# Performance work log

Hardware: AMD Instinct MI355X
Metric: run time of the kernel (lower is better)

Reference implementation:

```python
import jax, jax.numpy as jnp
import numpy as np

NEG_SLOPE = 0.2
EPS = 1e-16


def setup_inputs() -> dict:
    key = jax.random.key(0)
    k = jax.random.split(key, 6)
    N, K, D_IN, D_OUT = 20000, 32, 256, 256
    nodes = jax.random.normal(k[0], (N, D_IN), dtype=jnp.float32)
    neighbors = jax.random.normal(k[1], (N, K, D_IN), dtype=jnp.float32)
    # xavier-uniform-ish scales for faithfulness to init_params
    lim_w = float(np.sqrt(6.0 / (D_IN + D_OUT)))
    W = jax.random.uniform(k[2], (D_OUT, D_IN), minval=-lim_w, maxval=lim_w, dtype=jnp.float32)
    lim_a = float(np.sqrt(6.0 / (1 + D_OUT)))
    a_src = jax.random.uniform(k[3], (D_OUT,), minval=-lim_a, maxval=lim_a, dtype=jnp.float32)
    a_tgt = jax.random.uniform(k[4], (D_OUT,), minval=-lim_a, maxval=lim_a, dtype=jnp.float32)
    bias = jnp.zeros((D_OUT,), dtype=jnp.float32)
    return {"nodes": nodes, "neighbors": neighbors, "W": W, "a_src": a_src, "a_tgt": a_tgt, "bias": bias}


def reference(nodes, neighbors, W, a_src, a_tgt, bias):
    # GAT layer (num_of_heads=1), eval mode (dropout = identity).
    # nodes: [N, D_in], neighbors: [N, K, D_in]
    nodes_proj = nodes @ W.T                              # [N, D_out]
    scores_t = nodes_proj @ a_tgt                         # [N]
    neigh_proj = jnp.einsum('nkf,of->nko', neighbors, W)  # [N, K, D_out]
    scores_s = neigh_proj @ a_src                         # [N, K]
    e = scores_s + scores_t[:, None]                      # per-edge raw score
    e = jnp.where(e >= 0, e, NEG_SLOPE * e)               # leakyReLU(0.2)
    exp_e = jnp.exp(e)                                    # original uses raw exp (no max-subtract)
    attn = exp_e / (jnp.sum(exp_e, axis=1, keepdims=True) + EPS)  # [N, K]
    out = jnp.einsum('nk,nko->no', attn, neigh_proj)      # weighted sum over neighbors
    out = out + bias
    return jax.nn.elu(out)                                # activation = ELU
```

## Files before the change

### kernel.cpp

```cpp
#include <hip/hip_runtime.h>
#include <hip/hip_bf16.h>
#include <math.h>

#define D 256
#define KNB 32
#define NEG_SLOPE 0.2f

#define PART_OFF 53280
#define AGG_OFF  69664

using bfrag = __attribute__((ext_vector_type(8))) short;
using ffrag = __attribute__((ext_vector_type(4))) float;
using f32x4 = __attribute__((ext_vector_type(4))) float;

__device__ __forceinline__ unsigned short f2bf(float x) {
    __hip_bfloat16 h = __float2bfloat16(x);
    return *reinterpret_cast<unsigned short*>(&h);
}

__global__ __launch_bounds__(256) void prep1_kernel(
    const float* __restrict__ W, const float* __restrict__ a_src,
    const float* __restrict__ a_tgt, float* __restrict__ ws)
{
    int t = threadIdx.x;
    int b = blockIdx.x;
    if (b < 64) {
        float4 v = reinterpret_cast<const float4*>(W)[b * 256 + t];
        ushort4 u;
        u.x = f2bf(v.x); u.y = f2bf(v.y); u.z = f2bf(v.z); u.w = f2bf(v.w);
        reinterpret_cast<ushort4*>(ws + 512)[b * 256 + t] = u;
    } else {
        int bb = b - 64;
        float ps = 0.f, pt = 0.f;
        #pragma unroll
        for (int oo = 0; oo < 8; ++oo) {
            int o = bb * 8 + oo;
            float wv = W[o * D + t];
            ps = fmaf(a_src[o], wv, ps);
            pt = fmaf(a_tgt[o], wv, pt);
        }
        ws[PART_OFF + bb * 256 + t]        = ps;
        ws[PART_OFF + 8192 + bb * 256 + t] = pt;
    }
}

__global__ __launch_bounds__(256) void prep2_kernel(float* __restrict__ ws)
{
    int t = threadIdx.x;
    float s = 0.f, g = 0.f;
    #pragma unroll
    for (int j = 0; j < 32; ++j) {
        s += ws[PART_OFF + j * 256 + t];
        g += ws[PART_OFF + 8192 + j * 256 + t];
    }
    ws[t]     = s;
    ws[D + t] = g;
}

__global__ __launch_bounds__(256) void scores_t_kernel(
    const float* __restrict__ nodes, const float* __restrict__ ws,
    float* __restrict__ scores_t, int N)
{
    int wid  = threadIdx.x >> 6;
    int lane = threadIdx.x & 63;
    int n = blockIdx.x * 4 + wid;
    if (n >= N) return;
    f32x4 v = __builtin_nontemporal_load(
        reinterpret_cast<const f32x4*>(nodes + (size_t)n * D) + lane);
    float4 w = reinterpret_cast<const float4*>(ws + D)[lane];
    float s = v.x * w.x + v.y * w.y + v.z * w.z + v.w * w.w;
    #pragma unroll
    for (int off = 1; off < 64; off <<= 1) s += __shfl_xor(s, off);
    if (lane == 0) scores_t[n] = s;
}

__device__ __forceinline__ float xreduce8(const float* p, int lane)
{
    bool b0 = lane & 1, b1 = lane & 2, b2 = lane & 4;
    float s0_0 = (b0 ? p[1] : p[0]) + __shfl_xor(b0 ? p[0] : p[1], 1);
    float s0_1 = (b0 ? p[3] : p[2]) + __shfl_xor(b0 ? p[2] : p[3], 1);
    float s0_2 = (b0 ? p[5] : p[4]) + __shfl_xor(b0 ? p[4] : p[5], 1);
    float s0_3 = (b0 ? p[7] : p[6]) + __shfl_xor(b0 ? p[6] : p[7], 1);
    float s1_0 = (b1 ? s0_1 : s0_0) + __shfl_xor(b1 ? s0_0 : s0_1, 2);
    float s1_1 = (b1 ? s0_3 : s0_2) + __shfl_xor(b1 ? s0_2 : s0_3, 2);
    float s2   = (b2 ? s1_1 : s1_0) + __shfl_xor(b2 ? s1_0 : s1_1, 4);
    s2 += __shfl_xor(s2, 8);
    s2 += __shfl_xor(s2, 16);
    s2 += __shfl_xor(s2, 32);
    return s2;
}

__global__ __launch_bounds__(256) void attn_agg_kernel(
    const float* __restrict__ neighbors, const float* __restrict__ ws,
    const float* __restrict__ scores_t, unsigned short* __restrict__ aggbf, int N)
{
    __shared__ float spA[KNB], spB[KNB];
    __shared__ float wsumA[4], wsumB[4];
    __shared__ __align__(16) float4 part2A[4][64];
    __shared__ __align__(16) float4 part2B[4][64];

    const int t    = threadIdx.x;
    const int lane = t & 63;
    const int w    = t >> 6;
    const int nA   = blockIdx.x * 2;
    const bool hasB = (nA + 1 < N);
    const int nB   = hasB ? nA + 1 : nA;

    const float4 wsv = reinterpret_cast<const float4*>(ws)[lane];
    const float stA = scores_t[nA];
    const float stB = scores_t[nB];

    const f32x4* tA = reinterpret_cast<const f32x4*>(neighbors + (size_t)nA * (KNB * D));
    const f32x4* tB = reinterpret_cast<const f32x4*>(neighbors + (size_t)nB * (KNB * D));

    f32x4 vA[8], vB[8];
    #pragma unroll
    for (int i = 0; i < 8; ++i)
        vA[i] = __builtin_nontemporal_load(tA + (8 * w + i) * 64 + lane);
    #pragma unroll
    for (int i = 0; i < 8; ++i)
        vB[i] = __builtin_nontemporal_load(tB + (8 * w + i) * 64 + lane);

    {
        float p[8];
        #pragma unroll
        for (int i = 0; i < 8; ++i)
            p[i] = fmaf(vA[i].x, wsv.x, fmaf(vA[i].y, wsv.y,
                   fmaf(vA[i].z, wsv.z, vA[i].w * wsv.w)));
        float s2 = xreduce8(p, lane);
        float e = s2 + stA; e = (e >= 0.f) ? e : NEG_SLOPE * e;
        float x = __expf(e);
        float d = x + __shfl_xor(x, 1);
        d += __shfl_xor(d, 2);
        d += __shfl_xor(d, 4);
        if (lane < 8) spA[8 * w + lane] = x;
        if (lane == 0) wsumA[w] = d;
    }
    {
        float p[8];
        #pragma unroll
        for (int i = 0; i < 8; ++i)
            p[i] = fmaf(vB[i].x, wsv.x, fmaf(vB[i].y, wsv.y,
                   fmaf(vB[i].z, wsv.z, vB[i].w * wsv.w)));
        float s2 = xreduce8(p, lane);
        float e = s2 + stB; e = (e >= 0.f) ? e : NEG_SLOPE * e;
        float x = __expf(e);
        float d = x + __shfl_xor(x, 1);
        d += __shfl_xor(d, 2);
        d += __shfl_xor(d, 4);
        if (lane < 8) spB[8 * w + lane] = x;
        if (lane == 0) wsumB[w] = d;
    }
    __syncthreads();

    {
        float xw[8];
        #pragma unroll
        for (int i = 0; i < 8; ++i) xw[i] = spA[8 * w + i];
        float4 acc = make_float4(0.f, 0.f, 0.f, 0.f);
        #pragma unroll
        for (int i = 0; i < 8; ++i) {
            acc.x = fmaf(xw[i], vA[i].x, acc.x);
            acc.y = fmaf(xw[i], vA[i].y, acc.y);
            acc.z = fmaf(xw[i], vA[i].z, acc.z);
            acc.w = fmaf(xw[i], vA[i].w, acc.w);
        }
        part2A[w][lane] = acc;
    }
    {
        float xw[8];
        #pragma unroll
        for (int i = 0; i < 8; ++i) xw[i] = spB[8 * w + i];
        float4 acc = make_float4(0.f, 0.f, 0.f, 0.f);
        #pragma unroll
        for (int i = 0; i < 8; ++i) {
            acc.x = fmaf(xw[i], vB[i].x, acc.x);
            acc.y = fmaf(xw[i], vB[i].y, acc.y);
            acc.z = fmaf(xw[i], vB[i].z, acc.z);
            acc.w = fmaf(xw[i], vB[i].w, acc.w);
        }
        part2B[w][lane] = acc;
    }
    __syncthreads();

    if (w == 0) {
        float4 q0 = part2A[0][lane], q1 = part2A[1][lane];
        float4 q2 = part2A[2][lane], q3 = part2A[3][lane];
        float inv = 1.f / (wsumA[0] + wsumA[1] + wsumA[2] + wsumA[3] + 1e-16f);
        float4 r;
        r.x = (q0.x + q1.x + q2.x + q3.x) * inv;
        r.y = (q0.y + q1.y + q2.y + q3.y) * inv;
        r.z = (q0.z + q1.z + q2.z + q3.z) * inv;
        r.w = (q0.w + q1.w + q2.w + q3.w) * inv;
        ushort4 u;
        u.x = f2bf(r.x); u.y = f2bf(r.y); u.z = f2bf(r.z); u.w = f2bf(r.w);
        reinterpret_cast<ushort4*>(aggbf + (size_t)nA * D)[lane] = u;
    } else if (w == 1 && hasB) {
        float4 q0 = part2B[0][lane], q1 = part2B[1][lane];
        float4 q2 = part2B[2][lane], q3 = part2B[3][lane];
        float inv = 1.f / (wsumB[0] + wsumB[1] + wsumB[2] + wsumB[3] + 1e-16f);
        float4 r;
        r.x = (q0.x + q1.x + q2.x + q3.x) * inv;
        r.y = (q0.y + q1.y + q2.y + q3.y) * inv;
        r.z = (q0.z + q1.z + q2.z + q3.z) * inv;
        r.w = (q0.w + q1.w + q2.w + q3.w) * inv;
        ushort4 u;
        u.x = f2bf(r.x); u.y = f2bf(r.y); u.z = f2bf(r.z); u.w = f2bf(r.w);
        reinterpret_cast<ushort4*>(aggbf + (size_t)nB * D)[lane] = u;
    }
}

__global__ __launch_bounds__(64) void out_gemm_kernel(
    const unsigned short* __restrict__ aggbf,
    const unsigned short* __restrict__ wbf,
    const float* __restrict__ bias, float* __restrict__ out, int N)
{
    int l = threadIdx.x;
    int m0 = blockIdx.x * 16;
    if (m0 >= N) return;
    int lr = l & 15, lk = l >> 4;

    ffrag acc[16];
    #pragma unroll
    for (int nf = 0; nf < 16; ++nf) acc[nf] = ffrag{0.f, 0.f, 0.f, 0.f};

    #pragma unroll
    for (int ks = 0; ks < 8; ++ks) {
        bfrag a = *reinterpret_cast<const bfrag*>(
            aggbf + (size_t)(m0 + lr) * D + ks * 32 + lk * 8);
        #pragma unroll
        for (int nf = 0; nf < 16; ++nf) {
            bfrag b = *reinterpret_cast<const bfrag*>(
                wbf + (size_t)(nf * 16 + lr) * D + ks * 32 + lk * 8);
            acc[nf] = __builtin_amdgcn_mfma_f32_16x16x32_bf16(a, b, acc[nf], 0, 0, 0);
        }
    }

    #pragma unroll
    for (int nf = 0; nf < 16; ++nf) {
        int col = nf * 16 + lr;
        float bv = bias[col];
        #pragma unroll
        for (int r = 0; r < 4; ++r) {
            int m = m0 + lk * 4 + r;
            float x = acc[nf][r] + bv;
            x = (x > 0.f) ? x : expm1f(x);
            out[(size_t)m * D + col] = x;
        }
    }
}

extern "C" void kernel_launch(void* const* d_in, const int* in_sizes, int n_in,
                              void* d_out, int out_size, void* d_ws, size_t ws_size,
                              hipStream_t stream) {
    const float* nodes     = (const float*)d_in[0];
    const float* neighbors = (const float*)d_in[1];
    const float* W         = (const float*)d_in[2];
    const float* a_src     = (const float*)d_in[3];
    const float* a_tgt     = (const float*)d_in[4];
    const float* bias      = (const float*)d_in[5];
    float* out = (float*)d_out;
    float* ws  = (float*)d_ws;

    int N = in_sizes[0] / D;
    unsigned short* wbf   = (unsigned short*)(ws + 512);
    float* scores_t       = ws + 33280;
    unsigned short* aggbf = (unsigned short*)(ws + AGG_OFF);

    hipLaunchKernelGGL(prep1_kernel, dim3(96), dim3(256), 0, stream,
                       W, a_src, a_tgt, ws);
    hipLaunchKernelGGL(prep2_kernel, dim3(1), dim3(256), 0, stream, ws);
    hipLaunchKernelGGL(scores_t_kernel, dim3((N + 3) / 4), dim3(256), 0, stream,
                       nodes, ws, scores_t, N);
    hipLaunchKernelGGL(attn_agg_kernel, dim3((N + 1) / 2), dim3(256), 0, stream,
                       neighbors, ws, scores_t, aggbf, N);
    hipLaunchKernelGGL(out_gemm_kernel, dim3((N + 15) / 16), dim3(64), 0, stream,
                       aggbf, wbf, bias, out, N);
}
```

Measured before the change: 163.0 us.

## Make attention aggregation persistent with register double-buffered neighbor prefetch

The attention/aggregation kernel now runs a fixed grid of 2000 blocks. Each block walks nodes strided by the grid size and alternates two register buffers, so the next node's neighbor tile loads while the current one is scored and aggregated. The per-neighbor softmax weights are spread with wave shuffles instead of a shared-memory round trip, which removes one block barrier per node. The goal is to hide HBM latency on this bandwidth-bound stream and cut launch/tail overhead, at the cost of fewer resident blocks and a serial dependency inside each block.

```diff
diff --git a/kernel.cpp b/kernel.cpp
--- a/kernel.cpp
+++ b/kernel.cpp
@@ -5,6 +5,7 @@
 #define D 256
 #define KNB 32
 #define NEG_SLOPE 0.2f
+#define GRID_AGG 2000
 
 #define PART_OFF 53280
 #define AGG_OFF  69664
@@ -90,123 +91,120 @@
     return s2;
 }
 
+__device__ __forceinline__ void score_agg(
+    const f32x4* v, float st, const float4 wsv, int lane, int w,
+    float4 (*part2)[64], float* wsum)
+{
+    float p[8];
+    #pragma unroll
+    for (int i = 0; i < 8; ++i)
+        p[i] = fmaf(v[i].x, wsv.x, fmaf(v[i].y, wsv.y,
+               fmaf(v[i].z, wsv.z, v[i].w * wsv.w)));
+    float s2 = xreduce8(p, lane);
+    float e = s2 + st; e = (e >= 0.f) ? e : NEG_SLOPE * e;
+    float x = __expf(e);
+    float d = x + __shfl_xor(x, 1);
+    d += __shfl_xor(d, 2);
+    d += __shfl_xor(d, 4);
+    float xw[8];
+    int base = lane & 56;
+    #pragma unroll
+    for (int i = 0; i < 8; ++i) xw[i] = __shfl(x, base | i);
+    float4 acc = make_float4(0.f, 0.f, 0.f, 0.f);
+    #pragma unroll
+    for (int i = 0; i < 8; ++i) {
+        acc.x = fmaf(xw[i], v[i].x, acc.x);
+        acc.y = fmaf(xw[i], v[i].y, acc.y);
+        acc.z = fmaf(xw[i], v[i].z, acc.z);
+        acc.w = fmaf(xw[i], v[i].w, acc.w);
+    }
+    part2[w][lane] = acc;
+    if (lane == 0) wsum[w] = d;
+}
+
+__device__ __forceinline__ void finalize_node(
+    const float4 (*part2)[64], const float* wsum, int lane,
+    unsigned short* dst)
+{
+    float4 q0 = part2[0][lane], q1 = part2[1][lane];
+    float4 q2 = part2[2][lane], q3 = part2[3][lane];
+    float inv = 1.f / (wsum[0] + wsum[1] + wsum[2] + wsum[3] + 1e-16f);
+    float4 r;
+    r.x = (q0.x + q1.x + q2.x + q3.x) * inv;
+    r.y = (q0.y + q1.y + q2.y + q3.y) * inv;
+    r.z = (q0.z + q1.z + q2.z + q3.z) * inv;
+    r.w = (q0.w + q1.w + q2.w + q3.w) * inv;
+    ushort4 u;
+    u.x = f2bf(r.x); u.y = f2bf(r.y); u.z = f2bf(r.z); u.w = f2bf(r.w);
+    reinterpret_cast<ushort4*>(dst)[lane] = u;
+}
+
 __global__ __launch_bounds__(256) void attn_agg_kernel(
     const float* __restrict__ neighbors, const float* __restrict__ ws,
     const float* __restrict__ scores_t, unsigned short* __restrict__ aggbf, int N)
 {
-    __shared__ float spA[KNB], spB[KNB];
-    __shared__ float wsumA[4], wsumB[4];
-    __shared__ __align__(16) float4 part2A[4][64];
-    __shared__ __align__(16) float4 part2B[4][64];
+    __shared__ __align__(16) float4 part2[2][4][64];
+    __shared__ float wsum[2][4];
 
     const int t    = threadIdx.x;
     const int lane = t & 63;
     const int w    = t >> 6;
-    const int nA   = blockIdx.x * 2;
-    const bool hasB = (nA + 1 < N);
-    const int nB   = hasB ? nA + 1 : nA;
+    const int n0   = blockIdx.x;
+    const int GRID = GRID_AGG;
 
     const float4 wsv = reinterpret_cast<const float4*>(ws)[lane];
-    const float stA = scores_t[nA];
-    const float stB = scores_t[nB];
-
-    const f32x4* tA = reinterpret_cast<const f32x4*>(neighbors + (size_t)nA * (KNB * D));
-    const f32x4* tB = reinterpret_cast<const f32x4*>(neighbors + (size_t)nB * (KNB * D));
+
+    const int nd = (n0 < N) ? ((N - 1 - n0) / GRID + 1) : 0;
+    if (nd == 0) return;
 
     f32x4 vA[8], vB[8];
-    #pragma unroll
-    for (int i = 0; i < 8; ++i)
-        vA[i] = __builtin_nontemporal_load(tA + (8 * w + i) * 64 + lane);
-    #pragma unroll
-    for (int i = 0; i < 8; ++i)
-        vB[i] = __builtin_nontemporal_load(tB + (8 * w + i) * 64 + lane);
+    float stA = 0.f, stB = 0.f;
 
     {
-        float p[8];
+        const f32x4* tp = reinterpret_cast<const f32x4*>(
+            neighbors + (size_t)n0 * (KNB * D));
         #pragma unroll
         for (int i = 0; i < 8; ++i)
-            p[i] = fmaf(vA[i].x, wsv.x, fmaf(vA[i].y, wsv.y,
-                   fmaf(vA[i].z, wsv.z, vA[i].w * wsv.w)));
-        float s2 = xreduce8(p, lane);
-        float e = s2 + stA; e = (e >= 0.f) ? e : NEG_SLOPE * e;
-        float x = __expf(e);
-        float d = x + __shfl_xor(x, 1);
-        d += __shfl_xor(d, 2);
-        d += __shfl_xor(d, 4);
-        if (lane < 8) spA[8 * w + lane] = x;
-        if (lane == 0) wsumA[w] = d;
-    }
-    {
-        float p[8];
-        #pragma unroll
-        for (int i = 0; i < 8; ++i)
-            p[i] = fmaf(vB[i].x, wsv.x, fmaf(vB[i].y, wsv.y,
-                   fmaf(vB[i].z, wsv.z, vB[i].w * wsv.w)));
-        float s2 = xreduce8(p, lane);
-        float e = s2 + stB; e = (e >= 0.f) ? e : NEG_SLOPE * e;
-        float x = __expf(e);
-        float d = x + __shfl_xor(x, 1);
-        d += __shfl_xor(d, 2);
-        d += __shfl_xor(d, 4);
-        if (lane < 8) spB[8 * w + lane] = x;
-        if (lane == 0) wsumB[w] = d;
-    }
-    __syncthreads();
-
-    {
-        float xw[8];
-        #pragma unroll
-        for (int i = 0; i < 8; ++i) xw[i] = spA[8 * w + i];
-        float4 acc = make_float4(0.f, 0.f, 0.f, 0.f);
-        #pragma unroll
-        for (int i = 0; i < 8; ++i) {
-            acc.x = fmaf(xw[i], vA[i].x, acc.x);
-            acc.y = fmaf(xw[i], vA[i].y, acc.y);
-            acc.z = fmaf(xw[i], vA[i].z, acc.z);
-            acc.w = fmaf(xw[i], vA[i].w, acc.w);
-        }
-        part2A[w][lane] = acc;
-    }
-    {
-        float xw[8];
-        #pragma unroll
-        for (int i = 0; i < 8; ++i) xw[i] = spB[8 * w + i];
-        float4 acc = make_float4(0.f, 0.f, 0.f, 0.f);
-        #pragma unroll
-        for (int i = 0; i < 8; ++i) {
-            acc.x = fmaf(xw[i], vB[i].x, acc.x);
-            acc.y = fmaf(xw[i], vB[i].y, acc.y);
-            acc.z = fmaf(xw[i], vB[i].z, acc.z);
-            acc.w = fmaf(xw[i], vB[i].w, acc.w);
-        }
-        part2B[w][lane] = acc;
-    }
-    __syncthreads();
-
-    if (w == 0) {
-        float4 q0 = part2A[0][lane], q1 = part2A[1][lane];
-        float4 q2 = part2A[2][lane], q3 = part2A[3][lane];
-        float inv = 1.f / (wsumA[0] + wsumA[1] + wsumA[2] + wsumA[3] + 1e-16f);
-        float4 r;
-        r.x = (q0.x + q1.x + q2.x + q3.x) * inv;
-        r.y = (q0.y + q1.y + q2.y + q3.y) * inv;
-        r.z = (q0.z + q1.z + q2.z + q3.z) * inv;
-        r.w = (q0.w + q1.w + q2.w + q3.w) * inv;
-        ushort4 u;
-        u.x = f2bf(r.x); u.y = f2bf(r.y); u.z = f2bf(r.z); u.w = f2bf(r.w);
-        reinterpret_cast<ushort4*>(aggbf + (size_t)nA * D)[lane] = u;
-    } else if (w == 1 && hasB) {
-        float4 q0 = part2B[0][lane], q1 = part2B[1][lane];
-        float4 q2 = part2B[2][lane], q3 = part2B[3][lane];
-        float inv = 1.f / (wsumB[0] + wsumB[1] + wsumB[2] + wsumB[3] + 1e-16f);
-        float4 r;
-        r.x = (q0.x + q1.x + q2.x + q3.x) * inv;
-        r.y = (q0.y + q1.y + q2.y + q3.y) * inv;
-        r.z = (q0.z + q1.z + q2.z + q3.z) * inv;
-        r.w = (q0.w + q1.w + q2.w + q3.w) * inv;
-        ushort4 u;
-        u.x = f2bf(r.x); u.y = f2bf(r.y); u.z = f2bf(r.z); u.w = f2bf(r.w);
-        reinterpret_cast<ushort4*>(aggbf + (size_t)nB * D)[lane] = u;
+            vA[i] = __builtin_nontemporal_load(tp + (8 * w + i) * 64 + lane);
+        stA = scores_t[n0];
+    }
+
+    const int npairs = (nd + 1) >> 1;
+    for (int it = 0; it < npairs; ++it) {
+        const int idxA = 2 * it;
+        const int nA = n0 + idxA * GRID;
+        const int nB = nA + GRID;
+        const bool hasB  = (idxA + 1) < nd;
+        const bool hasA2 = (idxA + 2) < nd;
+
+        if (hasB) {
+            const f32x4* tp = reinterpret_cast<const f32x4*>(
+                neighbors + (size_t)nB * (KNB * D));
+            #pragma unroll
+            for (int i = 0; i < 8; ++i)
+                vB[i] = __builtin_nontemporal_load(tp + (8 * w + i) * 64 + lane);
+            stB = scores_t[nB];
+        }
+
+        score_agg(vA, stA, wsv, lane, w, part2[0], wsum[0]);
+        __syncthreads();
+        if (w == 0) finalize_node(part2[0], wsum[0], lane, aggbf + (size_t)nA * D);
+
+        if (hasA2) {
+            const int nA2 = nA + 2 * GRID;
+            const f32x4* tp = reinterpret_cast<const f32x4*>(
+                neighbors + (size_t)nA2 * (KNB * D));
+            #pragma unroll
+            for (int i = 0; i < 8; ++i)
+                vA[i] = __builtin_nontemporal_load(tp + (8 * w + i) * 64 + lane);
+            stA = scores_t[nA2];
+        }
+
+        if (hasB) {
+            score_agg(vB, stB, wsv, lane, w, part2[1], wsum[1]);
+            __syncthreads();
+            if (w == 1) finalize_node(part2[1], wsum[1], lane, aggbf + (size_t)nB * D);
+        }
     }
 }
 
@@ -272,7 +270,7 @@
     hipLaunchKernelGGL(prep2_kernel, dim3(1), dim3(256), 0, stream, ws);
     hipLaunchKernelGGL(scores_t_kernel, dim3((N + 3) / 4), dim3(256), 0, stream,
                        nodes, ws, scores_t, N);
-    hipLaunchKernelGGL(attn_agg_kernel, dim3((N + 1) / 2), dim3(256), 0, stream,
+    hipLaunchKernelGGL(attn_agg_kernel, dim3(GRID_AGG), dim3(256), 0, stream,
                        neighbors, ws, scores_t, aggbf, N);
     hipLaunchKernelGGL(out_gemm_kernel, dim3((N + 15) / 16), dim3(64), 0, stream,
                        aggbf, wbf, bias, out, N);
```

Measured after the change: 164.0 us. No clear change (+0.6%).
